# Kernel tuning notes

Hardware: AMD Instinct MI355X
Metric: run time of the kernel (lower is better)

The kernel has to match this reference:

```python
import jax, jax.numpy as jnp
import numpy as np

UNITS = 1024
D_MODEL = 1024
H = 16
DK = 64
DV = 64
M = 128
B = 4
S = 1024


def setup_inputs() -> dict:
    key = jax.random.key(0)
    ks = jax.random.split(key, 12)
    s = 1.0 / np.sqrt(D_MODEL)
    inp = {
        "queries": jax.random.normal(ks[0], (B, S, D_MODEL), jnp.float32),
        "keys": jax.random.normal(ks[1], (B, S, D_MODEL), jnp.float32),
        "values": jax.random.normal(ks[2], (B, S, D_MODEL), jnp.float32),
        "Wq": jax.random.normal(ks[3], (D_MODEL, H * DK), jnp.float32) * s,
        "bq": jnp.zeros((H * DK,), jnp.float32),
        "Wk": jax.random.normal(ks[4], (D_MODEL, H * DK), jnp.float32) * s,
        "bk": jnp.zeros((H * DK,), jnp.float32),
        "Wv": jax.random.normal(ks[5], (D_MODEL, H * DV), jnp.float32) * s,
        "bv": jnp.zeros((H * DV,), jnp.float32),
        "Wo": jax.random.normal(ks[6], (H * DV, UNITS), jnp.float32) * (1.0 / np.sqrt(H * DV)),
        "bo": jnp.zeros((UNITS,), jnp.float32),
        "mk": jax.random.normal(ks[7], (1, M, H * DK), jnp.float32) * 0.1,
        "mv": jax.random.normal(ks[8], (1, M, H * DV), jnp.float32) * 0.1,
        "h": H,
    }
    return inp


def reference(queries, keys, values, Wq, bq, Wk, bk, Wv, bv, Wo, bo, mk, mv, h):
    Bq, Sq, _ = queries.shape
    m = mk.shape[1]
    dk = Wk.shape[1] // h
    dv = Wv.shape[1] // h
    scale_m = jnp.sqrt(jnp.asarray(m, queries.dtype))

    # Q projection: [B, h, Sq, dk]
    q = (queries @ Wq + bq).reshape(Bq, Sq, h, dk).transpose(0, 2, 1, 3)

    # K/V projections with m learned memory slots concatenated on the seq axis
    k_flat = jnp.concatenate(
        [keys @ Wk + bk, scale_m * jnp.broadcast_to(mk, (Bq, m, h * dk))], axis=1
    )  # [B, Sk+m, h*dk]
    v_flat = jnp.concatenate(
        [values @ Wv + bv, scale_m * jnp.broadcast_to(mv, (Bq, m, h * dv))], axis=1
    )  # [B, Sk+m, h*dv]
    Skm = k_flat.shape[1]
    k = k_flat.reshape(Bq, Skm, h, dk).transpose(0, 2, 1, 3)  # [B, h, Sk+m, dk]
    v = v_flat.reshape(Bq, Skm, h, dv).transpose(0, 2, 1, 3)  # [B, h, Sk+m, dv]

    # Scaled dot-product attention over sequence + memory slots
    scores = jnp.einsum("bhqd,bhkd->bhqk", q, k) / jnp.sqrt(jnp.asarray(dk, q.dtype))
    attn = jax.nn.softmax(scores, axis=-1)  # [B, h, Sq, Sk+m]
    out = jnp.einsum("bhqk,bhkd->bhqd", attn, v)  # [B, h, Sq, dv]
    out = out.transpose(0, 2, 1, 3).reshape(Bq, Sq, h * dv)
    return out @ Wo + bo
```

## Files before the change

### kernel.cpp

```cpp
#include <hip/hip_runtime.h>

typedef __attribute__((ext_vector_type(8))) __bf16 bf16x8;
typedef __attribute__((ext_vector_type(4))) float f32x4;

#define DEVINL __device__ __forceinline__

constexpr int BZ = 4;
constexpr int SEQ = 1024;
constexpr int DMODEL = 1024;
constexpr int NH = 16;
constexpr int HD = 64;
constexpr int MSLOT = 128;
constexpr int NT = BZ * SEQ;
constexpr int SKM = SEQ + MSLOT;
constexpr int VT_LD = BZ * SKM;
constexpr float SCALE_M = 11.313708498984761f;
constexpr float SCEXP = 0.18033688011112042f;
constexpr size_t OF_QIN  = 0;
constexpr size_t OF_KIN  = OF_QIN  + (size_t)NT * DMODEL;
constexpr size_t OF_VIN  = OF_KIN  + (size_t)NT * DMODEL;
constexpr size_t OF_WQT  = OF_VIN  + (size_t)NT * DMODEL;
constexpr size_t OF_WKT  = OF_WQT  + (size_t)DMODEL * DMODEL;
constexpr size_t OF_WVT  = OF_WKT  + (size_t)DMODEL * DMODEL;
constexpr size_t OF_WOT  = OF_WVT  + (size_t)DMODEL * DMODEL;
constexpr size_t OF_QB   = OF_WOT  + (size_t)DMODEL * DMODEL;
constexpr size_t OF_KPR  = OF_QB   + (size_t)NT * DMODEL;
constexpr size_t OF_KMEM = OF_KPR  + (size_t)NT * DMODEL;
constexpr size_t OF_VTG  = OF_KMEM + (size_t)MSLOT * DMODEL;
constexpr size_t OF_AOUT = OF_VTG  + (size_t)DMODEL * VT_LD;

DEVINL unsigned short f2bf(float f) {
  union { float f; unsigned u; } v; v.f = f;
  unsigned r = v.u + 0x7FFF + ((v.u >> 16) & 1);
  return (unsigned short)(r >> 16);
}

#if __has_builtin(__builtin_amdgcn_cvt_pk_bf16_f32)
DEVINL unsigned pack2(float a, float b) {
  auto t = __builtin_amdgcn_cvt_pk_bf16_f32(a, b);
  unsigned r; __builtin_memcpy(&r, &t, 4); return r;
}
#else
DEVINL unsigned pack2(float a, float b) {
  return (unsigned)f2bf(a) | ((unsigned)f2bf(b) << 16);
}
#endif

#if __has_builtin(__builtin_amdgcn_exp2f)
DEVINL float fast_exp2(float x) { return __builtin_amdgcn_exp2f(x); }
#else
DEVINL float fast_exp2(float x) { return exp2f(x); }
#endif

DEVINL f32x4 mfma16(bf16x8 a, bf16x8 b, f32x4 c) {
  return __builtin_amdgcn_mfma_f32_16x16x32_bf16(a, b, c, 0, 0, 0);
}

DEVINL void gload16(const unsigned short* gp, unsigned short* lp) {
  __builtin_amdgcn_global_load_lds(
      (const __attribute__((address_space(1))) unsigned int*)(const void*)gp,
      (__attribute__((address_space(3))) unsigned int*)(void*)lp, 16, 0, 0);
}

__global__ __launch_bounds__(256) void prep_all(
    const float* __restrict__ q, const float* __restrict__ k, const float* __restrict__ v,
    const float* __restrict__ W0, const float* __restrict__ W1,
    const float* __restrict__ W2, const float* __restrict__ W3,
    const float* __restrict__ mk, const float* __restrict__ mv,
    unsigned short* __restrict__ dq, unsigned short* __restrict__ dk,
    unsigned short* __restrict__ dv,
    unsigned short* __restrict__ d0, unsigned short* __restrict__ d1,
    unsigned short* __restrict__ d2, unsigned short* __restrict__ d3,
    unsigned short* __restrict__ Kmm, unsigned short* __restrict__ VtG) {
  __shared__ float t[32][65];
  const int tid = threadIdx.x;
  const int bid = blockIdx.x;
  if (bid < 6144) {
    const int tz = bid >> 11;
    const float* src = (tz == 0) ? q : (tz == 1) ? k : v;
    unsigned short* dst = (tz == 0) ? dq : (tz == 1) ? dk : dv;
    int i = ((bid & 2047) * 256 + tid) * 8;
    float4 v0 = *(const float4*)(src + i);
    float4 v1 = *(const float4*)(src + i + 4);
    union { unsigned u2[4]; uint4 v; } o;
    o.u2[0] = pack2(v0.x, v0.y); o.u2[1] = pack2(v0.z, v0.w);
    o.u2[2] = pack2(v1.x, v1.y); o.u2[3] = pack2(v1.z, v1.w);
    *(uint4*)(dst + i) = o.v;
  } else if (bid < 8192) {
    const int rel = bid - 6144;
    const int z = rel >> 9, rem = rel & 511;
    const float* src = (z == 0) ? W0 : (z == 1) ? W1 : (z == 2) ? W2 : W3;
    unsigned short* dst = (z == 0) ? d0 : (z == 1) ? d1 : (z == 2) ? d2 : d3;
    const int n0 = (rem & 31) * 32, k0 = (rem >> 5) * 64;
    {
      int c = tid & 31, rg = tid >> 5;
#pragma unroll
      for (int rr = 0; rr < 8; ++rr)
        t[c][rg * 8 + rr] = src[(size_t)(k0 + rg * 8 + rr) * DMODEL + n0 + c];
    }
    __syncthreads();
    {
      int n = tid >> 3, ck = tid & 7;
      union { unsigned short u[8]; uint4 v; } o;
#pragma unroll
      for (int j = 0; j < 8; ++j) o.u[j] = f2bf(t[n][ck * 8 + j]);
      *(uint4*)(dst + (size_t)(n0 + n) * DMODEL + k0 + ck * 8) = o.v;
    }
  } else if (bid < 8704) {
    int i = (bid - 8192) * 256 + tid;
    Kmm[i] = f2bf(mk[i] * SCALE_M);
  } else {
    const int rel = bid - 8704;
    const int j0 = (rel & 3) * 32, c0 = (rel >> 2) * 32;
    const int tx = tid & 31, ty = tid >> 5;
#pragma unroll
    for (int r = 0; r < 4; ++r)
      t[ty + r * 8][tx] = mv[(size_t)(j0 + ty + r * 8) * DMODEL + c0 + tx];
    __syncthreads();
#pragma unroll
    for (int r = 0; r < 4; ++r) {
      int c = c0 + ty + r * 8;
      unsigned short vv = f2bf(t[tx][ty + r * 8] * SCALE_M);
#pragma unroll
      for (int bb = 0; bb < BZ; ++bb)
        VtG[(size_t)c * VT_LD + bb * SKM + SEQ + j0 + tx] = vv;
    }
  }
}

__global__ __launch_bounds__(256, 3) void proj_qkv(
    const unsigned short* __restrict__ Qin, const unsigned short* __restrict__ Kin,
    const unsigned short* __restrict__ Vin, const unsigned short* __restrict__ Wqt,
    const unsigned short* __restrict__ Wkt, const unsigned short* __restrict__ Wvt,
    const float* __restrict__ bq, const float* __restrict__ bk,
    const float* __restrict__ bv, unsigned short* __restrict__ Qbp,
    unsigned short* __restrict__ Kprp, unsigned short* __restrict__ VtG) {
  __shared__ unsigned short As0[128 * 32], As1[128 * 32];
  __shared__ unsigned short Bs0[128 * 32], Bs1[128 * 32];
  const int tid = threadIdx.x;
  const int pid = blockIdx.x >> 8;
  const int idx = blockIdx.x & 255;
  const int w = tid >> 6, lane = tid & 63, quad = lane >> 4, l16 = lane & 15;
  const int wr = w >> 1, wc = w & 1;
  const int mt = idx & 31, nt = idx >> 5;
  f32x4 acc[4][4] = {};

  const unsigned short* Abase;
  const unsigned short* Bbase;
  if (pid == 0)      { Abase = Qin + (size_t)(mt * 128) * DMODEL; Bbase = Wqt + (size_t)(nt * 128) * DMODEL; }
  else if (pid == 1) { Abase = Kin + (size_t)(mt * 128) * DMODEL; Bbase = Wkt + (size_t)(nt * 128) * DMODEL; }
  else               { Abase = Wvt + (size_t)(nt * 128) * DMODEL; Bbase = Vin + (size_t)(mt * 128) * DMODEL; }

  const int srow = tid >> 2, sslot = tid & 3;
  for (int kt = 0; kt < 16; ++kt) {
    const int k0 = kt * 64;
#pragma unroll
    for (int hb = 0; hb < 2; ++hb) {
      unsigned short* al = hb ? As1 : As0;
      unsigned short* bl = hb ? Bs1 : Bs0;
#pragma unroll
      for (int gi = 0; gi < 2; ++gi) {
        int g = gi * 256 + tid;
        int row = g >> 2, slot = g & 3;
        gload16(Abase + (size_t)row * DMODEL + k0 + hb * 32 + slot * 8, al + g * 8);
        gload16(Bbase + (size_t)row * DMODEL + k0 + hb * 32 + slot * 8, bl + g * 8);
      }
    }
    __syncthreads();
#pragma unroll
    for (int hb = 0; hb < 2; ++hb) {
      const unsigned short* al = hb ? As1 : As0;
      const unsigned short* bl = hb ? Bs1 : Bs0;
      bf16x8 af[4], bfr[4];
#pragma unroll
      for (int rb = 0; rb < 4; ++rb)
        af[rb] = *(const bf16x8*)(al + (wr * 64 + rb * 16 + l16) * 32 + quad * 8);
#pragma unroll
      for (int cb = 0; cb < 4; ++cb)
        bfr[cb] = *(const bf16x8*)(bl + (wc * 64 + cb * 16 + l16) * 32 + quad * 8);
#pragma unroll
      for (int rb = 0; rb < 4; ++rb)
#pragma unroll
        for (int cb = 0; cb < 4; ++cb)
          acc[rb][cb] = mfma16(af[rb], bfr[cb], acc[rb][cb]);
    }
    __syncthreads();
  }

  if (pid < 2) {
    const float* bias   = pid ? bk : bq;
    unsigned short* out = pid ? Kprp : Qbp;
    const float osc     = pid ? 1.0f : SCEXP;
    const int m0 = mt * 128, n0 = nt * 128;
#pragma unroll
    for (int rb = 0; rb < 4; ++rb)
#pragma unroll
      for (int cb = 0; cb < 4; ++cb)
#pragma unroll
        for (int r = 0; r < 4; ++r) {
          int row = m0 + wr * 64 + rb * 16 + quad * 4 + r;
          int col = n0 + wc * 64 + cb * 16 + l16;
          out[(size_t)row * DMODEL + col] = f2bf((acc[rb][cb][r] + bias[col]) * osc);
        }
  } else {
    const int t0 = mt * 128, n0 = nt * 128;
#pragma unroll
    for (int rb = 0; rb < 4; ++rb)
#pragma unroll
      for (int cb = 0; cb < 4; ++cb)
#pragma unroll
        for (int r = 0; r < 4; ++r) {
          int n = n0 + wr * 64 + rb * 16 + quad * 4 + r;
          int tok = t0 + wc * 64 + cb * 16 + l16;
          int col = tok + (tok >> 10) * MSLOT;
          VtG[(size_t)n * VT_LD + col] = f2bf(acc[rb][cb][r] + bv[n]);
        }
  }
}

__global__ __launch_bounds__(256) void gemm_out(const unsigned short* __restrict__ A,
                                                const unsigned short* __restrict__ Wt,
                                                const float* __restrict__ bias,
                                                float* __restrict__ Cout) {
  __shared__ unsigned short A0[64 * 32], A1[64 * 32];
  __shared__ unsigned short B0[64 * 32], B1[64 * 32];
  const int tid = threadIdx.x;
  const int idx = blockIdx.x;
  const int m0 = (idx & 63) * 64, n0 = (idx >> 6) * 64;
  const int w = tid >> 6, lane = tid & 63, quad = lane >> 4, l16 = lane & 15;
  const int wr = w >> 1, wc = w & 1;
  f32x4 acc[2][2] = {};
  const unsigned short* rA = A + (size_t)m0 * DMODEL;
  const unsigned short* rB = Wt + (size_t)n0 * DMODEL;
  const int srow = tid >> 2, sslot = tid & 3;
  for (int kt = 0; kt < 16; ++kt) {
    const int k0 = kt * 64;
    gload16(rA + (size_t)srow * DMODEL + k0 + sslot * 8, A0 + tid * 8);
    gload16(rA + (size_t)srow * DMODEL + k0 + 32 + sslot * 8, A1 + tid * 8);
    gload16(rB + (size_t)srow * DMODEL + k0 + sslot * 8, B0 + tid * 8);
    gload16(rB + (size_t)srow * DMODEL + k0 + 32 + sslot * 8, B1 + tid * 8);
    __syncthreads();
#pragma unroll
    for (int hb = 0; hb < 2; ++hb) {
      const unsigned short* al = hb ? A1 : A0;
      const unsigned short* bl = hb ? B1 : B0;
      bf16x8 af[2], bfr[2];
#pragma unroll
      for (int rb = 0; rb < 2; ++rb)
        af[rb] = *(const bf16x8*)(al + (wr * 32 + rb * 16 + l16) * 32 + quad * 8);
#pragma unroll
      for (int cb = 0; cb < 2; ++cb)
        bfr[cb] = *(const bf16x8*)(bl + (wc * 32 + cb * 16 + l16) * 32 + quad * 8);
#pragma unroll
      for (int rb = 0; rb < 2; ++rb)
#pragma unroll
        for (int cb = 0; cb < 2; ++cb)
          acc[rb][cb] = mfma16(af[rb], bfr[cb], acc[rb][cb]);
    }
    __syncthreads();
  }
#pragma unroll
  for (int rb = 0; rb < 2; ++rb)
#pragma unroll
    for (int cb = 0; cb < 2; ++cb)
#pragma unroll
      for (int r = 0; r < 4; ++r) {
        int row = m0 + wr * 32 + rb * 16 + quad * 4 + r;
        int col = n0 + wc * 32 + cb * 16 + l16;
        Cout[(size_t)row * DMODEL + col] = acc[rb][cb][r] + bias[col];
      }
}

__global__ __launch_bounds__(256) void attn_kernel(const unsigned short* __restrict__ Qb,
                                                   const unsigned short* __restrict__ Kproj,
                                                   const unsigned short* __restrict__ Kmem,
                                                   const unsigned short* __restrict__ VtG,
                                                   unsigned short* __restrict__ Aout) {
  __shared__ unsigned short Ks[2][64 * 64];
  __shared__ unsigned short Vs[2][64 * 64];
  __shared__ unsigned short Pl[4 * 16 * 64];
  const int tid = threadIdx.x;
  const int bh = blockIdx.x & 63, qb = blockIdx.x >> 6;
  const int b = bh & 3, h = bh >> 2;
  const int w = tid >> 6, lane = tid & 63, quad = lane >> 4, l16 = lane & 15;
  const int token0 = b * SEQ + qb * 64 + w * 16;
  unsigned short* Pw = Pl + w * 16 * 64;
  const int lx = l16 & 7;

  const int row0 = tid >> 3, slot0 = tid & 7;
  const int g1 = tid + 256;
  const int row1 = g1 >> 3, slot1 = g1 & 7;
  const int loff0 = row0 * 64 + (slot0 ^ (row0 & 7)) * 8;
  const int loff1 = row1 * 64 + (slot1 ^ (row1 & 7)) * 8;

  auto kbase = [&](int tile) -> const unsigned short* {
    return (tile < 16) ? Kproj + (size_t)(b * SEQ + tile * 64) * DMODEL + h * HD
                       : Kmem + (size_t)((tile - 16) * 64) * DMODEL + h * HD;
  };
  auto vbase = [&](int tile) -> const unsigned short* {
    int c0 = (tile < 16) ? b * SKM + tile * 64 : b * SKM + SEQ + (tile - 16) * 64;
    return VtG + (size_t)(h * HD) * VT_LD + c0;
  };

  bf16x8 qf[2];
#pragma unroll
  for (int t = 0; t < 2; ++t)
    qf[t] = *(const bf16x8*)(Qb + (size_t)(token0 + l16) * DMODEL + h * HD + t * 32 + quad * 8);

  bf16x8 ones;
  {
    union { unsigned short u[8]; bf16x8 v; } one8;
#pragma unroll
    for (int i = 0; i < 8; ++i) one8.u[i] = 0x3F80;
    ones = one8.v;
  }

  f32x4 O[4] = {};
  f32x4 Lacc = {};

  uint4 kr0, kr1, vr0, vr1;
  {
    const unsigned short* kp = kbase(0);
    const unsigned short* vp = vbase(0);
    kr0 = *(const uint4*)(kp + (size_t)row0 * DMODEL + slot0 * 8);
    kr1 = *(const uint4*)(kp + (size_t)row1 * DMODEL + slot1 * 8);
    vr0 = *(const uint4*)(vp + (size_t)row0 * VT_LD + slot0 * 8);
    vr1 = *(const uint4*)(vp + (size_t)row1 * VT_LD + slot1 * 8);
  }
  *(uint4*)(Ks[0] + loff0) = kr0;
  *(uint4*)(Ks[0] + loff1) = kr1;
  *(uint4*)(Vs[0] + loff0) = vr0;
  *(uint4*)(Vs[0] + loff1) = vr1;
  __syncthreads();

  for (int tile = 0; tile < 18; ++tile) {
    const int cur = tile & 1;
    if (tile < 17) {
      const unsigned short* kp = kbase(tile + 1);
      const unsigned short* vp = vbase(tile + 1);
      kr0 = *(const uint4*)(kp + (size_t)row0 * DMODEL + slot0 * 8);
      kr1 = *(const uint4*)(kp + (size_t)row1 * DMODEL + slot1 * 8);
      vr0 = *(const uint4*)(vp + (size_t)row0 * VT_LD + slot0 * 8);
      vr1 = *(const uint4*)(vp + (size_t)row1 * VT_LD + slot1 * 8);
    }

    f32x4 sc[4] = {};
#pragma unroll
    for (int c = 0; c < 4; ++c)
#pragma unroll
      for (int t = 0; t < 2; ++t) {
        bf16x8 kb = *(const bf16x8*)(Ks[cur] + (c * 16 + l16) * 64 +
                                     ((t * 4 + quad) ^ lx) * 8);
        sc[c] = mfma16(kb, qf[t], sc[c]);
      }

#pragma unroll
    for (int c = 0; c < 4; ++c) {
      float p0 = fast_exp2(sc[c][0]);
      float p1 = fast_exp2(sc[c][1]);
      float p2 = fast_exp2(sc[c][2]);
      float p3 = fast_exp2(sc[c][3]);
      union { unsigned u[2]; } pk;
      pk.u[0] = pack2(p0, p1);
      pk.u[1] = pack2(p2, p3);
      *(uint2*)(Pw + l16 * 64 + ((2 * c + (quad >> 1)) ^ lx) * 8 + (quad & 1) * 4) =
          *(uint2*)pk.u;
    }
    __builtin_amdgcn_wave_barrier();

#pragma unroll
    for (int t2 = 0; t2 < 2; ++t2) {
      bf16x8 pa = *(const bf16x8*)(Pw + l16 * 64 + ((t2 * 4 + quad) ^ lx) * 8);
      Lacc = mfma16(pa, ones, Lacc);
#pragma unroll
      for (int c2 = 0; c2 < 4; ++c2) {
        bf16x8 vb = *(const bf16x8*)(Vs[cur] + (c2 * 16 + l16) * 64 +
                                     ((t2 * 4 + quad) ^ lx) * 8);
        O[c2] = mfma16(pa, vb, O[c2]);
      }
    }

    if (tile < 17) {
      *(uint4*)(Ks[cur ^ 1] + loff0) = kr0;
      *(uint4*)(Ks[cur ^ 1] + loff1) = kr1;
      *(uint4*)(Vs[cur ^ 1] + loff0) = vr0;
      *(uint4*)(Vs[cur ^ 1] + loff1) = vr1;
    }
    __syncthreads();
  }

#pragma unroll
  for (int r = 0; r < 4; ++r) {
    float inv = 1.0f / Lacc[r];
#pragma unroll
    for (int c2 = 0; c2 < 4; ++c2)
      Aout[(size_t)(token0 + quad * 4 + r) * DMODEL + h * HD + c2 * 16 + l16] =
          f2bf(O[c2][r] * inv);
  }
}

extern "C" void kernel_launch(void* const* d_in, const int* in_sizes, int n_in,
                              void* d_out, int out_size, void* d_ws, size_t ws_size,
                              hipStream_t stream) {
  const float* queries = (const float*)d_in[0];
  const float* keys    = (const float*)d_in[1];
  const float* values  = (const float*)d_in[2];
  const float* Wq = (const float*)d_in[3];
  const float* bq = (const float*)d_in[4];
  const float* Wk = (const float*)d_in[5];
  const float* bk = (const float*)d_in[6];
  const float* Wv = (const float*)d_in[7];
  const float* bv = (const float*)d_in[8];
  const float* Wo = (const float*)d_in[9];
  const float* bo = (const float*)d_in[10];
  const float* mk = (const float*)d_in[11];
  const float* mv = (const float*)d_in[12];

  unsigned short* ws = (unsigned short*)d_ws;
  unsigned short* Qin  = ws + OF_QIN;
  unsigned short* Kin  = ws + OF_KIN;
  unsigned short* Vin  = ws + OF_VIN;
  unsigned short* Wqt  = ws + OF_WQT;
  unsigned short* Wkt  = ws + OF_WKT;
  unsigned short* Wvt  = ws + OF_WVT;
  unsigned short* Wot  = ws + OF_WOT;
  unsigned short* Qbp  = ws + OF_QB;
  unsigned short* Kprp = ws + OF_KPR;
  unsigned short* Kmm  = ws + OF_KMEM;
  unsigned short* VtGp = ws + OF_VTG;
  unsigned short* Aoutp = ws + OF_AOUT;

  prep_all<<<8832, 256, 0, stream>>>(queries, keys, values, Wq, Wk, Wv, Wo, mk, mv,
                                     Qin, Kin, Vin, Wqt, Wkt, Wvt, Wot, Kmm, VtGp);

  proj_qkv<<<768, 256, 0, stream>>>(Qin, Kin, Vin, Wqt, Wkt, Wvt, bq, bk, bv,
                                    Qbp, Kprp, VtGp);

  attn_kernel<<<1024, 256, 0, stream>>>(Qbp, Kprp, Kmm, VtGp, Aoutp);

  gemm_out<<<1024, 256, 0, stream>>>(Aoutp, Wot, bo, (float*)d_out);
}
```

Baseline: 211.1 us.

## Stage K/V tiles via direct global-to-LDS loads and raise MFMA wave priority

Replaces register-staged K/V prefetch (global load to registers, then LDS store after compute) with direct global-to-LDS loads issued into the alternate buffer, laying out the swizzle on the source side. This frees VGPRs and removes the LDS store instructions. It also brackets the MFMA sections with s_setprio to favour matrix-issuing waves. Correctness depends on the loads completing before the barrier.

```diff
diff --git a/kernel.cpp b/kernel.cpp
--- a/kernel.cpp
+++ b/kernel.cpp
@@ -287,11 +287,15 @@
   unsigned short* Pw = Pl + w * 16 * 64;
   const int lx = l16 & 7;
 
-  const int row0 = tid >> 3, slot0 = tid & 7;
-  const int g1 = tid + 256;
-  const int row1 = g1 >> 3, slot1 = g1 & 7;
-  const int loff0 = row0 * 64 + (slot0 ^ (row0 & 7)) * 8;
-  const int loff1 = row1 * 64 + (slot1 ^ (row1 & 7)) * 8;
+  const int ck0 = 2 * w, ck1 = 2 * w + 1;
+  const int lrow = lane >> 3;
+  const int lslot = (lane & 7) ^ lrow;
+  const size_t ksrc0 = (size_t)(8 * ck0 + lrow) * DMODEL + lslot * 8;
+  const size_t ksrc1 = (size_t)(8 * ck1 + lrow) * DMODEL + lslot * 8;
+  const size_t vsrc0 = (size_t)(8 * ck0 + lrow) * VT_LD + lslot * 8;
+  const size_t vsrc1 = (size_t)(8 * ck1 + lrow) * VT_LD + lslot * 8;
+  const int ldst0 = ck0 * 512 + lane * 8;
+  const int ldst1 = ck1 * 512 + lane * 8;
 
   auto kbase = [&](int tile) -> const unsigned short* {
     return (tile < 16) ? Kproj + (size_t)(b * SEQ + tile * 64) * DMODEL + h * HD
@@ -302,6 +306,15 @@
     return VtG + (size_t)(h * HD) * VT_LD + c0;
   };
 
+  auto stage = [&](int buf, int tile) {
+    const unsigned short* kp = kbase(tile);
+    const unsigned short* vp = vbase(tile);
+    gload16(kp + ksrc0, Ks[buf] + ldst0);
+    gload16(kp + ksrc1, Ks[buf] + ldst1);
+    gload16(vp + vsrc0, Vs[buf] + ldst0);
+    gload16(vp + vsrc1, Vs[buf] + ldst1);
+  };
+
   bf16x8 qf[2];
 #pragma unroll
   for (int t = 0; t < 2; ++t)
@@ -318,33 +331,15 @@
   f32x4 O[4] = {};
   f32x4 Lacc = {};
 
-  uint4 kr0, kr1, vr0, vr1;
-  {
-    const unsigned short* kp = kbase(0);
-    const unsigned short* vp = vbase(0);
-    kr0 = *(const uint4*)(kp + (size_t)row0 * DMODEL + slot0 * 8);
-    kr1 = *(const uint4*)(kp + (size_t)row1 * DMODEL + slot1 * 8);
-    vr0 = *(const uint4*)(vp + (size_t)row0 * VT_LD + slot0 * 8);
-    vr1 = *(const uint4*)(vp + (size_t)row1 * VT_LD + slot1 * 8);
-  }
-  *(uint4*)(Ks[0] + loff0) = kr0;
-  *(uint4*)(Ks[0] + loff1) = kr1;
-  *(uint4*)(Vs[0] + loff0) = vr0;
-  *(uint4*)(Vs[0] + loff1) = vr1;
+  stage(0, 0);
   __syncthreads();
 
   for (int tile = 0; tile < 18; ++tile) {
     const int cur = tile & 1;
-    if (tile < 17) {
-      const unsigned short* kp = kbase(tile + 1);
-      const unsigned short* vp = vbase(tile + 1);
-      kr0 = *(const uint4*)(kp + (size_t)row0 * DMODEL + slot0 * 8);
-      kr1 = *(const uint4*)(kp + (size_t)row1 * DMODEL + slot1 * 8);
-      vr0 = *(const uint4*)(vp + (size_t)row0 * VT_LD + slot0 * 8);
-      vr1 = *(const uint4*)(vp + (size_t)row1 * VT_LD + slot1 * 8);
-    }
+    if (tile < 17) stage(cur ^ 1, tile + 1);
 
     f32x4 sc[4] = {};
+    __builtin_amdgcn_s_setprio(1);
 #pragma unroll
     for (int c = 0; c < 4; ++c)
 #pragma unroll
@@ -353,6 +348,7 @@
                                      ((t * 4 + quad) ^ lx) * 8);
         sc[c] = mfma16(kb, qf[t], sc[c]);
       }
+    __builtin_amdgcn_s_setprio(0);
 
 #pragma unroll
     for (int c = 0; c < 4; ++c) {
@@ -368,6 +364,7 @@
     }
     __builtin_amdgcn_wave_barrier();
 
+    __builtin_amdgcn_s_setprio(1);
 #pragma unroll
     for (int t2 = 0; t2 < 2; ++t2) {
       bf16x8 pa = *(const bf16x8*)(Pw + l16 * 64 + ((t2 * 4 + quad) ^ lx) * 8);
@@ -379,13 +376,8 @@
         O[c2] = mfma16(pa, vb, O[c2]);
       }
     }
-
-    if (tile < 17) {
-      *(uint4*)(Ks[cur ^ 1] + loff0) = kr0;
-      *(uint4*)(Ks[cur ^ 1] + loff1) = kr1;
-      *(uint4*)(Vs[cur ^ 1] + loff0) = vr0;
-      *(uint4*)(Vs[cur ^ 1] + loff1) = vr1;
-    }
+    __builtin_amdgcn_s_setprio(0);
+
     __syncthreads();
   }
 
```

New measurement: 209.2 us. About the same (-0.9%).
